# Performance work log

Measured on AMD Instinct MI355X. Metric: run time of the kernel, lower is better.

The kernel has to match this reference:

```python
import jax, jax.numpy as jnp
import numpy as np

N = 10000      # nodes
E = 640000     # directed edges
D = 128        # feature width
C = 10         # classes
G = 64         # graphs in batch


def setup_inputs() -> dict:
    key = jax.random.key(0)
    ks = jax.random.split(key, 9)
    x = jax.random.normal(ks[0], (N, D), dtype=jnp.float32)
    edge_index = jax.random.randint(ks[1], (2, E), 0, N, dtype=jnp.int64)
    batch = jnp.sort(jax.random.randint(ks[2], (N,), 0, G, dtype=jnp.int64))
    scale = 1.0 / np.sqrt(D)
    W1 = jax.random.normal(ks[3], (D, D), dtype=jnp.float32) * scale
    W2 = jax.random.normal(ks[4], (D, D), dtype=jnp.float32) * scale
    W3 = jax.random.normal(ks[5], (D, D), dtype=jnp.float32) * scale
    W4 = jax.random.normal(ks[6], (D, D), dtype=jnp.float32) * scale
    fc_w = jax.random.normal(ks[7], (D, C), dtype=jnp.float32) * scale
    fc_b = jnp.zeros((C,), dtype=jnp.float32)
    return {"x": x, "edge_index": edge_index, "batch": batch,
            "W1": W1, "W2": W2, "W3": W3, "W4": W4,
            "fc_w": fc_w, "fc_b": fc_b}


def _gcn_conv(x, src, dst, deg_inv_sqrt, W):
    # GCNConv: h = x @ W; aggregate D^{-1/2}(A+I)D^{-1/2} h; then ReLU (activation).
    h = x @ W                                        # [N, D]
    norm = deg_inv_sqrt[src] * deg_inv_sqrt[dst]     # [E]
    msgs = h[src] * norm[:, None]                    # gather + scale
    agg = jax.ops.segment_sum(msgs, dst, num_segments=N)
    agg = agg + h * (deg_inv_sqrt * deg_inv_sqrt)[:, None]  # self-loop term
    return jax.nn.relu(agg)


def reference(x, edge_index, batch, W1, W2, W3, W4, fc_w, fc_b):
    src, dst = edge_index[0], edge_index[1]
    # degree counting self-loops (A + I normalization)
    deg = jax.ops.segment_sum(jnp.ones((E,), x.dtype), dst, num_segments=N) + 1.0
    deg_inv_sqrt = jax.lax.rsqrt(deg)
    for W in (W1, W2, W3, W4):
        x = _gcn_conv(x, src, dst, deg_inv_sqrt, W)
    xr = jax.ops.segment_sum(x, batch, num_segments=G)   # global_add_pool
    logits = x @ fc_w + fc_b
    return jax.nn.log_softmax(logits, axis=1), xr
```

## Files before the change

### kernel.cpp

```cpp
#include <hip/hip_runtime.h>
#include <math.h>

#define N_NODES 10000
#define N_EDGES 640000
#define DIM     128
#define NCLS    10
#define NGRAPH  64
#define NB      157
#define BCAP    4608
#define EPB     4000
#define NPB     8

typedef unsigned int uint32;
typedef unsigned short ushort16;

__device__ __forceinline__ ushort16 f32_to_bf16_rne(float f) {
    uint32 u = __float_as_uint(f);
    u = (u + 0x7fffu + ((u >> 16) & 1u)) >> 16;
    return (ushort16)u;
}

__device__ __forceinline__ float blo(uint32 x) { return __uint_as_float(x << 16); }
__device__ __forceinline__ float bhi(uint32 x) { return __uint_as_float(x & 0xffff0000u); }

__global__ __launch_bounds__(256) void binA_gemm1(const int* __restrict__ src,
                                                  const int* __restrict__ dst,
                                                  int* __restrict__ gcursor,
                                                  uint32* __restrict__ bins,
                                                  const float* __restrict__ X,
                                                  const float* __restrict__ W,
                                                  ushort16* __restrict__ Gh) {
    __shared__ uint32 pk[EPB];
    __shared__ int cntS[NB], offS[NB], curS[NB], gposS[NB];

    if (blockIdx.x < 625) {
        int c    = threadIdx.x & 127;
        int rg   = threadIdx.x >> 7;
        int row0 = blockIdx.x * 16 + rg * 8;
        const float* xb = X + row0 * DIM;
        float acc[8] = {0.f, 0.f, 0.f, 0.f, 0.f, 0.f, 0.f, 0.f};
        for (int k = 0; k < DIM; k += 4) {
            float w0 = W[(k + 0) * DIM + c];
            float w1 = W[(k + 1) * DIM + c];
            float w2 = W[(k + 2) * DIM + c];
            float w3 = W[(k + 3) * DIM + c];
#pragma unroll
            for (int r = 0; r < 8; r++) {
                float4 xv = *(const float4*)(xb + r * DIM + k);
                acc[r] += xv.x * w0 + xv.y * w1 + xv.z * w2 + xv.w * w3;
            }
        }
#pragma unroll
        for (int r = 0; r < 8; r++)
            Gh[(row0 + r) * DIM + c] = f32_to_bf16_rne(acc[r]);
        return;
    }

    int ab  = blockIdx.x - 625;
    int tid = threadIdx.x;
    for (int i = tid; i < NB; i += 256) cntS[i] = 0;
    __syncthreads();

    int base = ab * EPB;
    uint32 pr[16];
#pragma unroll
    for (int it = 0; it < 16; it++) {
        int i = it * 256 + tid;
        uint32 p = 0xffffffffu;
        if (i < EPB) {
            int e = base + i;
            p = ((uint32)dst[e] << 16) | (uint32)src[e];
            atomicAdd(&cntS[p >> 22], 1);
        }
        pr[it] = p;
    }
    __syncthreads();

    if (tid < 64) {
        int carry = 0;
        for (int r = 0; r < 3; r++) {
            int idx = r * 64 + tid;
            int v = (idx < NB) ? cntS[idx] : 0;
            int inc = v;
#pragma unroll
            for (int o = 1; o < 64; o <<= 1) {
                int u = __shfl_up(inc, o, 64);
                if (tid >= o) inc += u;
            }
            if (idx < NB) { offS[idx] = inc - v + carry; curS[idx] = inc - v + carry; }
            carry += __shfl(inc, 63, 64);
        }
    }
    __syncthreads();

#pragma unroll
    for (int it = 0; it < 16; it++) {
        uint32 p = pr[it];
        if (p != 0xffffffffu) {
            int b = p >> 22;
            pk[atomicAdd(&curS[b], 1)] = p;
        }
    }
    __syncthreads();

    if (tid < NB) gposS[tid] = atomicAdd(&gcursor[tid], cntS[tid]);
    __syncthreads();

#pragma unroll
    for (int it = 0; it < 16; it++) {
        int i = it * 256 + tid;
        if (i < EPB) {
            uint32 u = pk[i];
            int b = u >> 22;
            int gp = gposS[b] + (i - offS[b]);
            if (gp < BCAP) bins[b * BCAP + gp] = u;
        }
    }
}

__global__ __launch_bounds__(256) void binB(const int* __restrict__ gcursor,
                                            const uint32* __restrict__ bins,
                                            ushort16* __restrict__ col,
                                            int* __restrict__ deg,
                                            float* __restrict__ dis) {
    __shared__ ushort16 adj[64 * 128];
    __shared__ int cnt2[64];
    int b   = blockIdx.x;
    int tid = threadIdx.x;
    if (tid < 64) cnt2[tid] = 0;
    __syncthreads();
    int tc = gcursor[b];
    if (tc > BCAP) tc = BCAP;
    const uint32* bb = bins + b * BCAP;
    for (int i = tid; i < tc; i += 256) {
        uint32 u = bb[i];
        int local = (u >> 16) & 63;
        int r = atomicAdd(&cnt2[local], 1);
        if (r < 128) adj[(local << 7) + r] = (ushort16)(u & 0xffffu);
    }
    __syncthreads();
    uint4* dstp = (uint4*)(col + (size_t)b * 64 * 128);
    const uint4* srcp = (const uint4*)adj;
    for (int j = tid; j < 1024; j += 256) dstp[j] = srcp[j];
    if (tid < 64) {
        int node = b * 64 + tid;
        int c = cnt2[tid] < 128 ? cnt2[tid] : 128;
        deg[node] = c;
        dis[node] = rsqrtf((float)c + 1.0f);
    }
}

template <bool SCALED_IN>
__device__ __forceinline__ void agg_to_lds(const ushort16* __restrict__ Gh,
                                           const int* __restrict__ deg,
                                           const ushort16* __restrict__ col,
                                           const float* __restrict__ dis,
                                           float* __restrict__ Xs) {
    int tid  = threadIdx.x;
    int wave = tid >> 6;
    int lane = tid & 63;
    int grp  = lane >> 4;
    int sl   = lane & 15;
    const uint32* g32 = (const uint32*)Gh;
    const uint32* gp  = g32 + (sl << 2);

#pragma unroll
    for (int i = 0; i < 2; i++) {
        int vr = wave * 2 + i;
        int v  = blockIdx.x * NPB + vr;
        int dv = deg[v];
        uint32 colpack = ((const uint32*)(col + ((size_t)v << 7)))[lane];
        float acc[8];
#pragma unroll
        for (int j = 0; j < 8; j++) acc[j] = 0.f;

        int kk = 0;
        for (; kk + 8 <= dv; kk += 8) {
            int k0 = kk + grp, k1 = kk + 4 + grp;
            uint32 cp0 = __shfl(colpack, k0 >> 1, 64);
            uint32 cp1 = __shfl(colpack, k1 >> 1, 64);
            int u0 = (k0 & 1) ? (int)(cp0 >> 16) : (int)(cp0 & 0xffffu);
            int u1 = (k1 & 1) ? (int)(cp1 >> 16) : (int)(cp1 & 0xffffu);
            uint4 w0 = *(const uint4*)(gp + (u0 << 6));
            uint4 w1 = *(const uint4*)(gp + (u1 << 6));
            if (SCALED_IN) {
                acc[0] += blo(w0.x); acc[1] += bhi(w0.x);
                acc[2] += blo(w0.y); acc[3] += bhi(w0.y);
                acc[4] += blo(w0.z); acc[5] += bhi(w0.z);
                acc[6] += blo(w0.w); acc[7] += bhi(w0.w);
                acc[0] += blo(w1.x); acc[1] += bhi(w1.x);
                acc[2] += blo(w1.y); acc[3] += bhi(w1.y);
                acc[4] += blo(w1.z); acc[5] += bhi(w1.z);
                acc[6] += blo(w1.w); acc[7] += bhi(w1.w);
            } else {
                float s0 = dis[u0], s1 = dis[u1];
                acc[0] += s0 * blo(w0.x); acc[1] += s0 * bhi(w0.x);
                acc[2] += s0 * blo(w0.y); acc[3] += s0 * bhi(w0.y);
                acc[4] += s0 * blo(w0.z); acc[5] += s0 * bhi(w0.z);
                acc[6] += s0 * blo(w0.w); acc[7] += s0 * bhi(w0.w);
                acc[0] += s1 * blo(w1.x); acc[1] += s1 * bhi(w1.x);
                acc[2] += s1 * blo(w1.y); acc[3] += s1 * bhi(w1.y);
                acc[4] += s1 * blo(w1.z); acc[5] += s1 * bhi(w1.z);
                acc[6] += s1 * blo(w1.w); acc[7] += s1 * bhi(w1.w);
            }
        }
        for (; kk < dv; kk += 4) {
            int k = kk + grp;
            uint32 cp = __shfl(colpack, (k >> 1) & 63, 64);
            int u = (k & 1) ? (int)(cp >> 16) : (int)(cp & 0xffffu);
            if (k < dv) {
                uint4 w = *(const uint4*)(gp + (u << 6));
                float s = SCALED_IN ? 1.f : dis[u];
                acc[0] += s * blo(w.x); acc[1] += s * bhi(w.x);
                acc[2] += s * blo(w.y); acc[3] += s * bhi(w.y);
                acc[4] += s * blo(w.z); acc[5] += s * bhi(w.z);
                acc[6] += s * blo(w.w); acc[7] += s * bhi(w.w);
            }
        }
#pragma unroll
        for (int j = 0; j < 8; j++) {
            acc[j] += __shfl_xor(acc[j], 16, 64);
            acc[j] += __shfl_xor(acc[j], 32, 64);
        }
        float sv = dis[v];
        uint4 hs = *(const uint4*)(gp + (v << 6));
        float fs = SCALED_IN ? 1.f : sv;
        float r0 = sv * (acc[0] + fs * blo(hs.x));
        float r1 = sv * (acc[1] + fs * bhi(hs.x));
        float r2 = sv * (acc[2] + fs * blo(hs.y));
        float r3 = sv * (acc[3] + fs * bhi(hs.y));
        float r4 = sv * (acc[4] + fs * blo(hs.z));
        float r5 = sv * (acc[5] + fs * bhi(hs.z));
        float r6 = sv * (acc[6] + fs * blo(hs.w));
        float r7 = sv * (acc[7] + fs * bhi(hs.w));
        if (grp == 0) {
            float4* o = (float4*)(Xs + vr * DIM + sl * 8);
            o[0] = make_float4(fmaxf(r0, 0.f), fmaxf(r1, 0.f),
                               fmaxf(r2, 0.f), fmaxf(r3, 0.f));
            o[1] = make_float4(fmaxf(r4, 0.f), fmaxf(r5, 0.f),
                               fmaxf(r6, 0.f), fmaxf(r7, 0.f));
        }
    }
}

template <bool SCALED_IN>
__global__ __launch_bounds__(256) void fused_layer(const ushort16* __restrict__ Gh_in,
                                                   const int* __restrict__ deg,
                                                   const ushort16* __restrict__ col,
                                                   const float* __restrict__ dis,
                                                   const float* __restrict__ W,
                                                   ushort16* __restrict__ Gh_out) {
    __shared__ float Xs[NPB * DIM];
    agg_to_lds<SCALED_IN>(Gh_in, deg, col, dis, Xs);
    __syncthreads();

    int c  = threadIdx.x & 127;
    int rg = threadIdx.x >> 7;
    int row0 = blockIdx.x * NPB + rg * 4;
    float acc[4] = {0.f, 0.f, 0.f, 0.f};
    for (int k = 0; k < DIM; k += 4) {
        float w0 = W[(k + 0) * DIM + c];
        float w1 = W[(k + 1) * DIM + c];
        float w2 = W[(k + 2) * DIM + c];
        float w3 = W[(k + 3) * DIM + c];
#pragma unroll
        for (int r = 0; r < 4; r++) {
            float4 xv = *(const float4*)(Xs + (rg * 4 + r) * DIM + k);
            acc[r] += xv.x * w0 + xv.y * w1 + xv.z * w2 + xv.w * w3;
        }
    }
#pragma unroll
    for (int r = 0; r < 4; r++) {
        int row = row0 + r;
        Gh_out[row * DIM + c] = f32_to_bf16_rne(acc[r] * dis[row]);
    }
}

__global__ __launch_bounds__(256) void fused_last(const ushort16* __restrict__ Gh_in,
                                                  const int* __restrict__ deg,
                                                  const ushort16* __restrict__ col,
                                                  const float* __restrict__ dis,
                                                  const int* __restrict__ batch,
                                                  const float* __restrict__ fcw,
                                                  const float* __restrict__ fcb,
                                                  float* __restrict__ xr,
                                                  float* __restrict__ out) {
    __shared__ float Xs[NPB * DIM];
    agg_to_lds<true>(Gh_in, deg, col, dis, Xs);
    __syncthreads();

    int wave = threadIdx.x >> 6;
    int lane = threadIdx.x & 63;
#pragma unroll
    for (int i = 0; i < 2; i++) {
        int vr   = wave * 2 + i;
        int node = blockIdx.x * NPB + vr;
        float xl = Xs[vr * DIM + lane];
        float xh = Xs[vr * DIM + 64 + lane];
        float lg[NCLS];
#pragma unroll
        for (int c2 = 0; c2 < NCLS; c2++) {
            float p = xl * fcw[lane * NCLS + c2] + xh * fcw[(lane + 64) * NCLS + c2];
#pragma unroll
            for (int off = 32; off >= 1; off >>= 1) p += __shfl_xor(p, off, 64);
            lg[c2] = p + fcb[c2];
        }
        float m = lg[0];
#pragma unroll
        for (int c2 = 1; c2 < NCLS; c2++) m = fmaxf(m, lg[c2]);
        float s = 0.f;
#pragma unroll
        for (int c2 = 0; c2 < NCLS; c2++) s += expf(lg[c2] - m);
        float lse = m + logf(s);
        if (lane < NCLS) out[node * NCLS + lane] = lg[lane] - lse;
    }

    if (threadIdx.x < 128) {
        int start = blockIdx.x * NPB;
        int t = threadIdx.x;
        int b = batch[start];
        float a = 0.f;
        for (int n = 0; n < NPB; n++) {
            int bn = batch[start + n];
            if (bn != b) { atomicAdd(&xr[b * DIM + t], a); a = 0.f; b = bn; }
            a += Xs[n * DIM + t];
        }
        atomicAdd(&xr[b * DIM + t], a);
    }
}


extern "C" void kernel_launch(void* const* d_in, const int* in_sizes, int n_in,
                              void* d_out, int out_size, void* d_ws, size_t ws_size,
                              hipStream_t stream) {
    const float* x     = (const float*)d_in[0];
    const int*   ei    = (const int*)d_in[1];
    const int*   src   = ei;
    const int*   dst   = ei + N_EDGES;
    const int*   batch = (const int*)d_in[2];
    const float* W[4]  = {(const float*)d_in[3], (const float*)d_in[4],
                          (const float*)d_in[5], (const float*)d_in[6]};
    const float* fcw   = (const float*)d_in[7];
    const float* fcb   = (const float*)d_in[8];

    float* out_ls = (float*)d_out;
    float* out_xr = out_ls + N_NODES * NCLS;

    int*      gcursor = (int*)d_ws;
    int*      deg     = gcursor + 256;
    float*    dis     = (float*)(deg + 10240);
    uint32*   bins    = (uint32*)(dis + 10240);
    ushort16* col     = (ushort16*)(bins + NB * BCAP);
    ushort16* Gh_a    = col + (size_t)NB * 64 * 128;
    ushort16* Gh_b    = Gh_a + (size_t)N_NODES * DIM;

    hipMemsetAsync(gcursor, 0, 256 * sizeof(int), stream);
    hipMemsetAsync(out_xr, 0, NGRAPH * DIM * sizeof(float), stream);

    binA_gemm1<<<785, 256, 0, stream>>>(src, dst, gcursor, bins, x, W[0], Gh_a);
    binB      <<<NB, 256, 0, stream>>>(gcursor, bins, col, deg, dis);

    fused_layer<false><<<N_NODES / NPB, 256, 0, stream>>>(Gh_a, deg, col, dis, W[1], Gh_b);
    fused_layer<true> <<<N_NODES / NPB, 256, 0, stream>>>(Gh_b, deg, col, dis, W[2], Gh_a);
    fused_layer<true> <<<N_NODES / NPB, 256, 0, stream>>>(Gh_a, deg, col, dis, W[3], Gh_b);
    fused_last        <<<N_NODES / NPB, 256, 0, stream>>>(Gh_b, deg, col, dis, batch,
                                                          fcw, fcb, out_xr, out_ls);
}
```

Measured before the change: 198.3 us.

## Switch intermediates to fp16 with fdot2 math, split binning, fold memset

Stores the hidden features as fp16 instead of bf16 and does the neighbour accumulation with v_dot2 (fdot2), using selector constants or packed per-node scale values. The later-layer weights are repacked to fp16 pairs inside the first kernel so the dense products can also use fdot2. The main gather loop is unrolled to 16 neighbours to keep more loads in flight. binB is split into two blocks per bin, and the xr zeroing moves from a memset into the first kernel. fp16 has a narrower range than bf16 and adds rounding error, and the fp16 scale values affect accuracy.

New measurement: 182.2 us. 1.09x faster.

```diff
diff --git a/kernel.cpp b/kernel.cpp
--- a/kernel.cpp
+++ b/kernel.cpp
@@ -1,4 +1,5 @@
 #include <hip/hip_runtime.h>
+#include <hip/hip_fp16.h>
 #include <math.h>
 
 #define N_NODES 10000
@@ -13,15 +14,30 @@
 
 typedef unsigned int uint32;
 typedef unsigned short ushort16;
-
-__device__ __forceinline__ ushort16 f32_to_bf16_rne(float f) {
-    uint32 u = __float_as_uint(f);
-    u = (u + 0x7fffu + ((u >> 16) & 1u)) >> 16;
-    return (ushort16)u;
-}
-
-__device__ __forceinline__ float blo(uint32 x) { return __uint_as_float(x << 16); }
-__device__ __forceinline__ float bhi(uint32 x) { return __uint_as_float(x & 0xffff0000u); }
+typedef _Float16 h2v __attribute__((ext_vector_type(2)));
+
+#define SEL_LO 0x00003C00u
+#define SEL_HI 0x3C000000u
+
+__device__ __forceinline__ h2v as_h2(uint32 u) { h2v r; __builtin_memcpy(&r, &u, 4); return r; }
+
+__device__ __forceinline__ float fd2(uint32 w, uint32 p, float acc) {
+#if __has_builtin(__builtin_amdgcn_fdot2)
+    return __builtin_amdgcn_fdot2(as_h2(w), as_h2(p), acc, false);
+#else
+    h2v a = as_h2(w), b = as_h2(p);
+    return acc + (float)a[0] * (float)b[0] + (float)a[1] * (float)b[1];
+#endif
+}
+__device__ __forceinline__ float f16lo(uint32 u) { return (float)as_h2(u)[0]; }
+__device__ __forceinline__ float f16hi(uint32 u) { return (float)as_h2(u)[1]; }
+__device__ __forceinline__ ushort16 f32_f16(float f) {
+    return __half_as_ushort(__float2half(f));
+}
+__device__ __forceinline__ uint32 pack_f16x2(float lo, float hi) {
+    __half2 h = __floats2half2_rn(lo, hi);
+    uint32 u; __builtin_memcpy(&u, &h, 4); return u;
+}
 
 __global__ __launch_bounds__(256) void binA_gemm1(const int* __restrict__ src,
                                                   const int* __restrict__ dst,
@@ -29,7 +45,12 @@
                                                   uint32* __restrict__ bins,
                                                   const float* __restrict__ X,
                                                   const float* __restrict__ W,
-                                                  ushort16* __restrict__ Gh) {
+                                                  const float* __restrict__ W2,
+                                                  const float* __restrict__ W3,
+                                                  const float* __restrict__ W4,
+                                                  uint32* __restrict__ Wp,
+                                                  ushort16* __restrict__ Gh,
+                                                  float* __restrict__ xr) {
     __shared__ uint32 pk[EPB];
     __shared__ int cntS[NB], offS[NB], curS[NB], gposS[NB];
 
@@ -52,7 +73,25 @@
         }
 #pragma unroll
         for (int r = 0; r < 8; r++)
-            Gh[(row0 + r) * DIM + c] = f32_to_bf16_rne(acc[r]);
+            Gh[(row0 + r) * DIM + c] = f32_f16(acc[r]);
+        return;
+    }
+
+    if (blockIdx.x >= 786) {
+        int w = blockIdx.x - 786;
+        const float* Ws = (w == 0) ? W2 : (w == 1) ? W3 : W4;
+        uint32* Wd = Wp + w * (64 * DIM);
+        for (int i = threadIdx.x; i < 64 * DIM; i += 256) {
+            int k2 = i >> 7, c = i & 127;
+            Wd[i] = pack_f16x2(Ws[(2 * k2) * DIM + c], Ws[(2 * k2 + 1) * DIM + c]);
+        }
+        return;
+    }
+
+    if (blockIdx.x == 785) {
+        float4 z = make_float4(0.f, 0.f, 0.f, 0.f);
+        for (int j = threadIdx.x; j < NGRAPH * DIM / 4; j += 256)
+            ((float4*)xr)[j] = z;
         return;
     }
 
@@ -118,16 +157,18 @@
     }
 }
 
-__global__ __launch_bounds__(256) void binB(const int* __restrict__ gcursor,
-                                            const uint32* __restrict__ bins,
-                                            ushort16* __restrict__ col,
-                                            int* __restrict__ deg,
-                                            float* __restrict__ dis) {
-    __shared__ ushort16 adj[64 * 128];
-    __shared__ int cnt2[64];
-    int b   = blockIdx.x;
-    int tid = threadIdx.x;
-    if (tid < 64) cnt2[tid] = 0;
+__global__ __launch_bounds__(256) void binB2(const int* __restrict__ gcursor,
+                                             const uint32* __restrict__ bins,
+                                             ushort16* __restrict__ col,
+                                             int* __restrict__ deg,
+                                             float* __restrict__ dis,
+                                             uint32* __restrict__ disPh) {
+    __shared__ ushort16 adj[32 * 128];
+    __shared__ int cnt2[32];
+    int b    = blockIdx.x >> 1;
+    int half = blockIdx.x & 1;
+    int tid  = threadIdx.x;
+    if (tid < 32) cnt2[tid] = 0;
     __syncthreads();
     int tc = gcursor[b];
     if (tc > BCAP) tc = BCAP;
@@ -135,27 +176,33 @@
     for (int i = tid; i < tc; i += 256) {
         uint32 u = bb[i];
         int local = (u >> 16) & 63;
-        int r = atomicAdd(&cnt2[local], 1);
-        if (r < 128) adj[(local << 7) + r] = (ushort16)(u & 0xffffu);
-    }
-    __syncthreads();
-    uint4* dstp = (uint4*)(col + (size_t)b * 64 * 128);
+        if ((local >> 5) == half) {
+            int l5 = local & 31;
+            int r = atomicAdd(&cnt2[l5], 1);
+            if (r < 128) adj[(l5 << 7) + r] = (ushort16)(u & 0xffffu);
+        }
+    }
+    __syncthreads();
+    uint4* dstp = (uint4*)(col + (size_t)b * 64 * 128 + half * 32 * 128);
     const uint4* srcp = (const uint4*)adj;
-    for (int j = tid; j < 1024; j += 256) dstp[j] = srcp[j];
-    if (tid < 64) {
-        int node = b * 64 + tid;
+    for (int j = tid; j < 512; j += 256) dstp[j] = srcp[j];
+    if (tid < 32) {
+        int node = b * 64 + half * 32 + tid;
         int c = cnt2[tid] < 128 ? cnt2[tid] : 128;
+        float dv = rsqrtf((float)c + 1.0f);
         deg[node] = c;
-        dis[node] = rsqrtf((float)c + 1.0f);
-    }
-}
-
-template <bool SCALED_IN>
+        dis[node] = dv;
+        disPh[node] = (uint32)__half_as_ushort(__float2half(dv));
+    }
+}
+
+template <bool SCALED_IN, bool PACK_OUT>
 __device__ __forceinline__ void agg_to_lds(const ushort16* __restrict__ Gh,
                                            const int* __restrict__ deg,
                                            const ushort16* __restrict__ col,
                                            const float* __restrict__ dis,
-                                           float* __restrict__ Xs) {
+                                           const uint32* __restrict__ disPh,
+                                           void* __restrict__ Xout) {
     int tid  = threadIdx.x;
     int wave = tid >> 6;
     int lane = tid & 63;
@@ -175,6 +222,58 @@
         for (int j = 0; j < 8; j++) acc[j] = 0.f;
 
         int kk = 0;
+        for (; kk + 16 <= dv; kk += 16) {
+            int k0 = kk + grp, k1 = kk + 4 + grp, k2 = kk + 8 + grp, k3 = kk + 12 + grp;
+            uint32 cp0 = __shfl(colpack, k0 >> 1, 64);
+            uint32 cp1 = __shfl(colpack, k1 >> 1, 64);
+            uint32 cp2 = __shfl(colpack, k2 >> 1, 64);
+            uint32 cp3 = __shfl(colpack, k3 >> 1, 64);
+            int u0 = (k0 & 1) ? (int)(cp0 >> 16) : (int)(cp0 & 0xffffu);
+            int u1 = (k1 & 1) ? (int)(cp1 >> 16) : (int)(cp1 & 0xffffu);
+            int u2 = (k2 & 1) ? (int)(cp2 >> 16) : (int)(cp2 & 0xffffu);
+            int u3 = (k3 & 1) ? (int)(cp3 >> 16) : (int)(cp3 & 0xffffu);
+            uint4 w0 = *(const uint4*)(gp + (u0 << 6));
+            uint4 w1 = *(const uint4*)(gp + (u1 << 6));
+            uint4 w2 = *(const uint4*)(gp + (u2 << 6));
+            uint4 w3 = *(const uint4*)(gp + (u3 << 6));
+            if (SCALED_IN) {
+                acc[0] = fd2(w0.x, SEL_LO, acc[0]); acc[1] = fd2(w0.x, SEL_HI, acc[1]);
+                acc[2] = fd2(w0.y, SEL_LO, acc[2]); acc[3] = fd2(w0.y, SEL_HI, acc[3]);
+                acc[4] = fd2(w0.z, SEL_LO, acc[4]); acc[5] = fd2(w0.z, SEL_HI, acc[5]);
+                acc[6] = fd2(w0.w, SEL_LO, acc[6]); acc[7] = fd2(w0.w, SEL_HI, acc[7]);
+                acc[0] = fd2(w1.x, SEL_LO, acc[0]); acc[1] = fd2(w1.x, SEL_HI, acc[1]);
+                acc[2] = fd2(w1.y, SEL_LO, acc[2]); acc[3] = fd2(w1.y, SEL_HI, acc[3]);
+                acc[4] = fd2(w1.z, SEL_LO, acc[4]); acc[5] = fd2(w1.z, SEL_HI, acc[5]);
+                acc[6] = fd2(w1.w, SEL_LO, acc[6]); acc[7] = fd2(w1.w, SEL_HI, acc[7]);
+                acc[0] = fd2(w2.x, SEL_LO, acc[0]); acc[1] = fd2(w2.x, SEL_HI, acc[1]);
+                acc[2] = fd2(w2.y, SEL_LO, acc[2]); acc[3] = fd2(w2.y, SEL_HI, acc[3]);
+                acc[4] = fd2(w2.z, SEL_LO, acc[4]); acc[5] = fd2(w2.z, SEL_HI, acc[5]);
+                acc[6] = fd2(w2.w, SEL_LO, acc[6]); acc[7] = fd2(w2.w, SEL_HI, acc[7]);
+                acc[0] = fd2(w3.x, SEL_LO, acc[0]); acc[1] = fd2(w3.x, SEL_HI, acc[1]);
+                acc[2] = fd2(w3.y, SEL_LO, acc[2]); acc[3] = fd2(w3.y, SEL_HI, acc[3]);
+                acc[4] = fd2(w3.z, SEL_LO, acc[4]); acc[5] = fd2(w3.z, SEL_HI, acc[5]);
+                acc[6] = fd2(w3.w, SEL_LO, acc[6]); acc[7] = fd2(w3.w, SEL_HI, acc[7]);
+            } else {
+                uint32 dp0 = disPh[u0], dp1 = disPh[u1], dp2 = disPh[u2], dp3 = disPh[u3];
+                uint32 dq0 = dp0 << 16, dq1 = dp1 << 16, dq2 = dp2 << 16, dq3 = dp3 << 16;
+                acc[0] = fd2(w0.x, dp0, acc[0]); acc[1] = fd2(w0.x, dq0, acc[1]);
+                acc[2] = fd2(w0.y, dp0, acc[2]); acc[3] = fd2(w0.y, dq0, acc[3]);
+                acc[4] = fd2(w0.z, dp0, acc[4]); acc[5] = fd2(w0.z, dq0, acc[5]);
+                acc[6] = fd2(w0.w, dp0, acc[6]); acc[7] = fd2(w0.w, dq0, acc[7]);
+                acc[0] = fd2(w1.x, dp1, acc[0]); acc[1] = fd2(w1.x, dq1, acc[1]);
+                acc[2] = fd2(w1.y, dp1, acc[2]); acc[3] = fd2(w1.y, dq1, acc[3]);
+                acc[4] = fd2(w1.z, dp1, acc[4]); acc[5] = fd2(w1.z, dq1, acc[5]);
+                acc[6] = fd2(w1.w, dp1, acc[6]); acc[7] = fd2(w1.w, dq1, acc[7]);
+                acc[0] = fd2(w2.x, dp2, acc[0]); acc[1] = fd2(w2.x, dq2, acc[1]);
+                acc[2] = fd2(w2.y, dp2, acc[2]); acc[3] = fd2(w2.y, dq2, acc[3]);
+                acc[4] = fd2(w2.z, dp2, acc[4]); acc[5] = fd2(w2.z, dq2, acc[5]);
+                acc[6] = fd2(w2.w, dp2, acc[6]); acc[7] = fd2(w2.w, dq2, acc[7]);
+                acc[0] = fd2(w3.x, dp3, acc[0]); acc[1] = fd2(w3.x, dq3, acc[1]);
+                acc[2] = fd2(w3.y, dp3, acc[2]); acc[3] = fd2(w3.y, dq3, acc[3]);
+                acc[4] = fd2(w3.z, dp3, acc[4]); acc[5] = fd2(w3.z, dq3, acc[5]);
+                acc[6] = fd2(w3.w, dp3, acc[6]); acc[7] = fd2(w3.w, dq3, acc[7]);
+            }
+        }
         for (; kk + 8 <= dv; kk += 8) {
             int k0 = kk + grp, k1 = kk + 4 + grp;
             uint32 cp0 = __shfl(colpack, k0 >> 1, 64);
@@ -183,26 +282,18 @@
             int u1 = (k1 & 1) ? (int)(cp1 >> 16) : (int)(cp1 & 0xffffu);
             uint4 w0 = *(const uint4*)(gp + (u0 << 6));
             uint4 w1 = *(const uint4*)(gp + (u1 << 6));
-            if (SCALED_IN) {
-                acc[0] += blo(w0.x); acc[1] += bhi(w0.x);
-                acc[2] += blo(w0.y); acc[3] += bhi(w0.y);
-                acc[4] += blo(w0.z); acc[5] += bhi(w0.z);
-                acc[6] += blo(w0.w); acc[7] += bhi(w0.w);
-                acc[0] += blo(w1.x); acc[1] += bhi(w1.x);
-                acc[2] += blo(w1.y); acc[3] += bhi(w1.y);
-                acc[4] += blo(w1.z); acc[5] += bhi(w1.z);
-                acc[6] += blo(w1.w); acc[7] += bhi(w1.w);
-            } else {
-                float s0 = dis[u0], s1 = dis[u1];
-                acc[0] += s0 * blo(w0.x); acc[1] += s0 * bhi(w0.x);
-                acc[2] += s0 * blo(w0.y); acc[3] += s0 * bhi(w0.y);
-                acc[4] += s0 * blo(w0.z); acc[5] += s0 * bhi(w0.z);
-                acc[6] += s0 * blo(w0.w); acc[7] += s0 * bhi(w0.w);
-                acc[0] += s1 * blo(w1.x); acc[1] += s1 * bhi(w1.x);
-                acc[2] += s1 * blo(w1.y); acc[3] += s1 * bhi(w1.y);
-                acc[4] += s1 * blo(w1.z); acc[5] += s1 * bhi(w1.z);
-                acc[6] += s1 * blo(w1.w); acc[7] += s1 * bhi(w1.w);
-            }
+            uint32 dp0 = SCALED_IN ? SEL_LO : disPh[u0];
+            uint32 dp1 = SCALED_IN ? SEL_LO : disPh[u1];
+            uint32 dq0 = SCALED_IN ? SEL_HI : (dp0 << 16);
+            uint32 dq1 = SCALED_IN ? SEL_HI : (dp1 << 16);
+            acc[0] = fd2(w0.x, dp0, acc[0]); acc[1] = fd2(w0.x, dq0, acc[1]);
+            acc[2] = fd2(w0.y, dp0, acc[2]); acc[3] = fd2(w0.y, dq0, acc[3]);
+            acc[4] = fd2(w0.z, dp0, acc[4]); acc[5] = fd2(w0.z, dq0, acc[5]);
+            acc[6] = fd2(w0.w, dp0, acc[6]); acc[7] = fd2(w0.w, dq0, acc[7]);
+            acc[0] = fd2(w1.x, dp1, acc[0]); acc[1] = fd2(w1.x, dq1, acc[1]);
+            acc[2] = fd2(w1.y, dp1, acc[2]); acc[3] = fd2(w1.y, dq1, acc[3]);
+            acc[4] = fd2(w1.z, dp1, acc[4]); acc[5] = fd2(w1.z, dq1, acc[5]);
+            acc[6] = fd2(w1.w, dp1, acc[6]); acc[7] = fd2(w1.w, dq1, acc[7]);
         }
         for (; kk < dv; kk += 4) {
             int k = kk + grp;
@@ -210,11 +301,12 @@
             int u = (k & 1) ? (int)(cp >> 16) : (int)(cp & 0xffffu);
             if (k < dv) {
                 uint4 w = *(const uint4*)(gp + (u << 6));
-                float s = SCALED_IN ? 1.f : dis[u];
-                acc[0] += s * blo(w.x); acc[1] += s * bhi(w.x);
-                acc[2] += s * blo(w.y); acc[3] += s * bhi(w.y);
-                acc[4] += s * blo(w.z); acc[5] += s * bhi(w.z);
-                acc[6] += s * blo(w.w); acc[7] += s * bhi(w.w);
+                uint32 dp = SCALED_IN ? SEL_LO : disPh[u];
+                uint32 dq = SCALED_IN ? SEL_HI : (dp << 16);
+                acc[0] = fd2(w.x, dp, acc[0]); acc[1] = fd2(w.x, dq, acc[1]);
+                acc[2] = fd2(w.y, dp, acc[2]); acc[3] = fd2(w.y, dq, acc[3]);
+                acc[4] = fd2(w.z, dp, acc[4]); acc[5] = fd2(w.z, dq, acc[5]);
+                acc[6] = fd2(w.w, dp, acc[6]); acc[7] = fd2(w.w, dq, acc[7]);
             }
         }
 #pragma unroll
@@ -225,20 +317,30 @@
         float sv = dis[v];
         uint4 hs = *(const uint4*)(gp + (v << 6));
         float fs = SCALED_IN ? 1.f : sv;
-        float r0 = sv * (acc[0] + fs * blo(hs.x));
-        float r1 = sv * (acc[1] + fs * bhi(hs.x));
-        float r2 = sv * (acc[2] + fs * blo(hs.y));
-        float r3 = sv * (acc[3] + fs * bhi(hs.y));
-        float r4 = sv * (acc[4] + fs * blo(hs.z));
-        float r5 = sv * (acc[5] + fs * bhi(hs.z));
-        float r6 = sv * (acc[6] + fs * blo(hs.w));
-        float r7 = sv * (acc[7] + fs * bhi(hs.w));
+        float r0 = sv * (acc[0] + fs * f16lo(hs.x));
+        float r1 = sv * (acc[1] + fs * f16hi(hs.x));
+        float r2 = sv * (acc[2] + fs * f16lo(hs.y));
+        float r3 = sv * (acc[3] + fs * f16hi(hs.y));
+        float r4 = sv * (acc[4] + fs * f16lo(hs.z));
+        float r5 = sv * (acc[5] + fs * f16hi(hs.z));
+        float r6 = sv * (acc[6] + fs * f16lo(hs.w));
+        float r7 = sv * (acc[7] + fs * f16hi(hs.w));
         if (grp == 0) {
-            float4* o = (float4*)(Xs + vr * DIM + sl * 8);
-            o[0] = make_float4(fmaxf(r0, 0.f), fmaxf(r1, 0.f),
-                               fmaxf(r2, 0.f), fmaxf(r3, 0.f));
-            o[1] = make_float4(fmaxf(r4, 0.f), fmaxf(r5, 0.f),
-                               fmaxf(r6, 0.f), fmaxf(r7, 0.f));
+            if (PACK_OUT) {
+                uint32* o = (uint32*)Xout + vr * 64 + sl * 4;
+                uint4 pk4;
+                pk4.x = pack_f16x2(fmaxf(r0, 0.f), fmaxf(r1, 0.f));
+                pk4.y = pack_f16x2(fmaxf(r2, 0.f), fmaxf(r3, 0.f));
+                pk4.z = pack_f16x2(fmaxf(r4, 0.f), fmaxf(r5, 0.f));
+                pk4.w = pack_f16x2(fmaxf(r6, 0.f), fmaxf(r7, 0.f));
+                *(uint4*)o = pk4;
+            } else {
+                float4* o = (float4*)((float*)Xout + vr * DIM + sl * 8);
+                o[0] = make_float4(fmaxf(r0, 0.f), fmaxf(r1, 0.f),
+                                   fmaxf(r2, 0.f), fmaxf(r3, 0.f));
+                o[1] = make_float4(fmaxf(r4, 0.f), fmaxf(r5, 0.f),
+                                   fmaxf(r6, 0.f), fmaxf(r7, 0.f));
+            }
         }
     }
 }
@@ -248,31 +350,36 @@
                                                    const int* __restrict__ deg,
                                                    const ushort16* __restrict__ col,
                                                    const float* __restrict__ dis,
-                                                   const float* __restrict__ W,
+                                                   const uint32* __restrict__ disPh,
+                                                   const uint32* __restrict__ Wp,
                                                    ushort16* __restrict__ Gh_out) {
-    __shared__ float Xs[NPB * DIM];
-    agg_to_lds<SCALED_IN>(Gh_in, deg, col, dis, Xs);
+    __shared__ __align__(16) uint32 Xh[NPB * 64];
+    agg_to_lds<SCALED_IN, true>(Gh_in, deg, col, dis, disPh, Xh);
     __syncthreads();
 
     int c  = threadIdx.x & 127;
     int rg = threadIdx.x >> 7;
     int row0 = blockIdx.x * NPB + rg * 4;
+    const uint4* Xh4 = (const uint4*)Xh;
     float acc[4] = {0.f, 0.f, 0.f, 0.f};
-    for (int k = 0; k < DIM; k += 4) {
-        float w0 = W[(k + 0) * DIM + c];
-        float w1 = W[(k + 1) * DIM + c];
-        float w2 = W[(k + 2) * DIM + c];
-        float w3 = W[(k + 3) * DIM + c];
+    for (int q = 0; q < 16; q++) {
+        uint32 wp0 = Wp[(4 * q + 0) * DIM + c];
+        uint32 wp1 = Wp[(4 * q + 1) * DIM + c];
+        uint32 wp2 = Wp[(4 * q + 2) * DIM + c];
+        uint32 wp3 = Wp[(4 * q + 3) * DIM + c];
 #pragma unroll
         for (int r = 0; r < 4; r++) {
-            float4 xv = *(const float4*)(Xs + (rg * 4 + r) * DIM + k);
-            acc[r] += xv.x * w0 + xv.y * w1 + xv.z * w2 + xv.w * w3;
+            uint4 xv = Xh4[(rg * 4 + r) * 16 + q];
+            acc[r] = fd2(xv.x, wp0, acc[r]);
+            acc[r] = fd2(xv.y, wp1, acc[r]);
+            acc[r] = fd2(xv.z, wp2, acc[r]);
+            acc[r] = fd2(xv.w, wp3, acc[r]);
         }
     }
 #pragma unroll
     for (int r = 0; r < 4; r++) {
         int row = row0 + r;
-        Gh_out[row * DIM + c] = f32_to_bf16_rne(acc[r] * dis[row]);
+        Gh_out[row * DIM + c] = f32_f16(acc[r] * dis[row]);
     }
 }
 
@@ -280,13 +387,14 @@
                                                   const int* __restrict__ deg,
                                                   const ushort16* __restrict__ col,
                                                   const float* __restrict__ dis,
+                                                  const uint32* __restrict__ disPh,
                                                   const int* __restrict__ batch,
                                                   const float* __restrict__ fcw,
                                                   const float* __restrict__ fcb,
                                                   float* __restrict__ xr,
                                                   float* __restrict__ out) {
     __shared__ float Xs[NPB * DIM];
-    agg_to_lds<true>(Gh_in, deg, col, dis, Xs);
+    agg_to_lds<true, false>(Gh_in, deg, col, dis, disPh, Xs);
     __syncthreads();
 
     int wave = threadIdx.x >> 6;
@@ -338,8 +446,10 @@
     const int*   src   = ei;
     const int*   dst   = ei + N_EDGES;
     const int*   batch = (const int*)d_in[2];
-    const float* W[4]  = {(const float*)d_in[3], (const float*)d_in[4],
-                          (const float*)d_in[5], (const float*)d_in[6]};
+    const float* W1    = (const float*)d_in[3];
+    const float* W2    = (const float*)d_in[4];
+    const float* W3    = (const float*)d_in[5];
+    const float* W4    = (const float*)d_in[6];
     const float* fcw   = (const float*)d_in[7];
     const float* fcb   = (const float*)d_in[8];
 
@@ -353,16 +463,21 @@
     ushort16* col     = (ushort16*)(bins + NB * BCAP);
     ushort16* Gh_a    = col + (size_t)NB * 64 * 128;
     ushort16* Gh_b    = Gh_a + (size_t)N_NODES * DIM;
+    uint32*   Wp      = (uint32*)(Gh_b + (size_t)N_NODES * DIM);
+    uint32*   disPh   = Wp + 3 * 64 * DIM;
 
     hipMemsetAsync(gcursor, 0, 256 * sizeof(int), stream);
-    hipMemsetAsync(out_xr, 0, NGRAPH * DIM * sizeof(float), stream);
-
-    binA_gemm1<<<785, 256, 0, stream>>>(src, dst, gcursor, bins, x, W[0], Gh_a);
-    binB      <<<NB, 256, 0, stream>>>(gcursor, bins, col, deg, dis);
-
-    fused_layer<false><<<N_NODES / NPB, 256, 0, stream>>>(Gh_a, deg, col, dis, W[1], Gh_b);
-    fused_layer<true> <<<N_NODES / NPB, 256, 0, stream>>>(Gh_b, deg, col, dis, W[2], Gh_a);
-    fused_layer<true> <<<N_NODES / NPB, 256, 0, stream>>>(Gh_a, deg, col, dis, W[3], Gh_b);
-    fused_last        <<<N_NODES / NPB, 256, 0, stream>>>(Gh_b, deg, col, dis, batch,
-                                                          fcw, fcb, out_xr, out_ls);
-}
+
+    binA_gemm1<<<789, 256, 0, stream>>>(src, dst, gcursor, bins, x, W1,
+                                        W2, W3, W4, Wp, Gh_a, out_xr);
+    binB2     <<<2 * NB, 256, 0, stream>>>(gcursor, bins, col, deg, dis, disPh);
+
+    fused_layer<false><<<N_NODES / NPB, 256, 0, stream>>>(Gh_a, deg, col, dis, disPh,
+                                                          Wp, Gh_b);
+    fused_layer<true> <<<N_NODES / NPB, 256, 0, stream>>>(Gh_b, deg, col, dis, disPh,
+                                                          Wp + 64 * DIM, Gh_a);
+    fused_layer<true> <<<N_NODES / NPB, 256, 0, stream>>>(Gh_a, deg, col, dis, disPh,
+                                                          Wp + 2 * 64 * DIM, Gh_b);
+    fused_last        <<<N_NODES / NPB, 256, 0, stream>>>(Gh_b, deg, col, dis, disPh,
+                                                          batch, fcw, fcb, out_xr, out_ls);
+}
```
